# Optimization experiments

Measured on AMD Instinct MI355X. Metric: run time of the kernel, lower is better.

Reference implementation:

```python
import jax, jax.numpy as jnp
import numpy as np

EPS = 1e-08   # CanberraDistLayer eps (max(1e-8, 1e-8))
N_POW = 1.0   # similarity exponent
MAX_DIST = 1000000.0


def setup_inputs() -> dict:
    key = jax.random.key(0)
    k1, k2, k3, k4 = jax.random.split(key, 4)
    B, D_IN, H, OUT = 1024, 1024, 512, 512
    x = jax.random.normal(k1, (B, D_IN), dtype=jnp.float32)
    W1 = jax.random.normal(k2, (H, D_IN), dtype=jnp.float32) * 0.02  # MLP weight (torch Linear layout [out,in])
    b1 = jax.random.normal(k3, (H,), dtype=jnp.float32) * 0.02
    Wd = jax.random.normal(k4, (OUT, H), dtype=jnp.float32)          # dist-layer prototype rows
    return {"x": x, "W1": W1, "b1": b1, "Wd": Wd}


def reference(x, W1, b1, Wd):
    # MLP trunk: Linear + ReLU  -> hidden features h: [B, H]
    h = jax.nn.relu(jnp.einsum("bd,hd->bh", x, W1) + b1)
    # Canberra distance (variant='standard') of each hidden vector vs each weight row.
    # Broadcast to [B, OUT, H]; reduce over feature dim H.
    he = h[:, None, :]          # [B, 1, H]
    we = Wd[None, :, :]         # [1, OUT, H]
    numerator = jnp.abs(he - we)
    denominator = jnp.abs(he) + jnp.abs(we)
    denominator = jnp.where(denominator < EPS, EPS, denominator)
    canberra_dist = jnp.sum(numerator / denominator, axis=-1)  # [B, OUT]
    # scale=False path
    dist_clamped = jnp.clip(canberra_dist + EPS, EPS, MAX_DIST)
    similarity = dist_clamped ** (-N_POW)
    return similarity
```

## Files before the change

### kernel.cpp

```cpp
#include <hip/hip_runtime.h>
#include <hip/hip_fp16.h>

#define DIN 1024
#define H_SZ 512
#define OUT_SZ 512
#define EPSF 1e-8f

typedef __attribute__((ext_vector_type(8))) short short8v;
typedef __attribute__((ext_vector_type(4))) float f32x4;
typedef _Float16 half2v __attribute__((ext_vector_type(2)));

static __device__ inline void canb2f(unsigned hu, unsigned wu, unsigned& a) {
    unsigned mn, sm, y;
    asm("v_pk_min_f16 %0, %1, %2" : "=v"(mn) : "v"(hu), "v"(wu));
    asm("v_pk_add_f16 %0, %1, %2" : "=v"(sm) : "v"(hu), "v"(wu));
    y = 0x77997799u - sm;
    asm("v_pk_fma_f16 %0, %1, %2, %0" : "+v"(a) : "v"(mn), "v"(y));
}

static __device__ inline unsigned cvtpk(float lo, float hi) {
    unsigned u;
    asm("v_cvt_pk_bf16_f32 %0, %1, %2" : "=v"(u) : "v"(lo), "v"(hi));
    return u;
}

__global__ __launch_bounds__(512, 4) void gemm10(const float* __restrict__ x,
                                                 const float* __restrict__ W1,
                                                 const float* __restrict__ b1,
                                                 const float* __restrict__ Wd,
                                                 unsigned short* __restrict__ hh,
                                                 unsigned short* __restrict__ wh) {
    __shared__ unsigned short As[2][2][32][72];
    __shared__ unsigned short Bs[2][2][32][72];
    __shared__ float red[4][64][4];
    const int t  = threadIdx.x;

    const int flat = blockIdx.x + 32 * blockIdx.y;
    const int xcd  = flat & 7;
    const int idx  = flat >> 3;
    const int bt   = (xcd >> 1) * 8 + (idx & 7);
    const int ot   = (xcd & 1) * 8 + (idx >> 3);
    const int b0 = bt * 32;
    const int o0 = ot * 32;

    const int w  = t >> 6;
    const int l  = t & 63;
    const int q  = w & 3;
    const int kh = w >> 2;
    const int m0 = (q >> 1) * 16;
    const int n0 = (q & 1) * 16;
    const int lr = l & 15;
    const int lk = (l >> 4) * 8;
    const int th = t & 255;
    const int ar = th >> 3;
    const int ko = (th & 7) * 8;

    f32x4 acc = {0.f, 0.f, 0.f, 0.f};
    const float* arow = &x [(size_t)(b0 + ar) * DIN + kh * 512 + ko];
    const float* brow = &W1[(size_t)(o0 + ar) * DIN + kh * 512 + ko];

    float4 pa0[2], pa1[2], pb0[2], pb1[2];
    #pragma unroll
    for (int i = 0; i < 2; ++i) {
        pa0[i] = *reinterpret_cast<const float4*>(arow + i * 64);
        pa1[i] = *reinterpret_cast<const float4*>(arow + i * 64 + 4);
        pb0[i] = *reinterpret_cast<const float4*>(brow + i * 64);
        pb1[i] = *reinterpret_cast<const float4*>(brow + i * 64 + 4);
    }

    #pragma unroll
    for (int it = 0; it < 8; ++it) {
        const int sl  = it & 1;
        uint4 av, bv;
        av.x = cvtpk(pa0[sl].x, pa0[sl].y);
        av.y = cvtpk(pa0[sl].z, pa0[sl].w);
        av.z = cvtpk(pa1[sl].x, pa1[sl].y);
        av.w = cvtpk(pa1[sl].z, pa1[sl].w);
        bv.x = cvtpk(pb0[sl].x, pb0[sl].y);
        bv.y = cvtpk(pb0[sl].z, pb0[sl].w);
        bv.z = cvtpk(pb1[sl].x, pb1[sl].y);
        bv.w = cvtpk(pb1[sl].z, pb1[sl].w);
        *reinterpret_cast<uint4*>(&As[kh][sl][ar][ko]) = av;
        *reinterpret_cast<uint4*>(&Bs[kh][sl][ar][ko]) = bv;
        __syncthreads();
        if (it + 2 < 8) {
            pa0[sl] = *reinterpret_cast<const float4*>(arow + (it + 2) * 64);
            pa1[sl] = *reinterpret_cast<const float4*>(arow + (it + 2) * 64 + 4);
            pb0[sl] = *reinterpret_cast<const float4*>(brow + (it + 2) * 64);
            pb1[sl] = *reinterpret_cast<const float4*>(brow + (it + 2) * 64 + 4);
        }
        #pragma unroll
        for (int s = 0; s < 2; ++s) {
            const short8v af = *reinterpret_cast<const short8v*>(&As[kh][sl][m0 + lr][s * 32 + lk]);
            const short8v bf = *reinterpret_cast<const short8v*>(&Bs[kh][sl][n0 + lr][s * 32 + lk]);
            acc = __builtin_amdgcn_mfma_f32_16x16x32_bf16(af, bf, acc, 0, 0, 0);
        }
    }
    __syncthreads();
    if (kh == 1) {
        #pragma unroll
        for (int r = 0; r < 4; ++r) red[q][l][r] = acc[r];
    }
    __syncthreads();
    if (kh == 0) {
        const int col = o0 + n0 + lr;
        const float bias = b1[col];
        #pragma unroll
        for (int r = 0; r < 4; ++r) {
            const float v = acc[r] + red[q][l][r] + bias;
            const int m = b0 + m0 + (l >> 4) * 4 + r;
            hh[(size_t)m * H_SZ + col] = __half_as_ushort(__float2half(fmaxf(v, 0.0f)));
        }
    }
    const int gid = flat * 512 + t;
    const float wv0 = Wd[gid];
    wh[gid] = __half_as_ushort(__float2half(wv0 > 0.f ? wv0 : 0.f));
}

__global__ __launch_bounds__(512, 8) void canberra7(const unsigned short* __restrict__ hh,
                                                    const unsigned short* __restrict__ wh,
                                                    float* __restrict__ out) {
    __shared__ unsigned hs[32][132];
    __shared__ unsigned ws[16][132];
    const int t  = threadIdx.x;
    const int b0 = blockIdx.x * 32;
    const int o0 = blockIdx.y * 16;
    const unsigned* hu = reinterpret_cast<const unsigned*>(hh);
    const unsigned* wu = reinterpret_cast<const unsigned*>(wh);

    const int ks = t >> 6;
    const int l  = t & 63;
    const int bi = l >> 3;
    const int oj = l & 7;

    unsigned acc[4][2] = {};

    for (int ch = 0; ch < 2; ++ch) {
        if (ch) __syncthreads();
        #pragma unroll
        for (int r = 0; r < 2; ++r) {
            const int s = t + r * 512;
            const int row = s >> 5;
            const int c4  = s & 31;
            *reinterpret_cast<uint4*>(&hs[row][c4 * 4]) =
                *reinterpret_cast<const uint4*>(&hu[(size_t)(b0 + row) * 256 + ch * 128 + c4 * 4]);
        }
        {
            const int row = t >> 5;
            const int c4  = t & 31;
            *reinterpret_cast<uint4*>(&ws[row][c4 * 4]) =
                *reinterpret_cast<const uint4*>(&wu[(size_t)(o0 + row) * 256 + ch * 128 + c4 * 4]);
        }
        __syncthreads();

        #pragma unroll
        for (int g = 0; g < 4; ++g) {
            const int col = ks * 16 + g * 4;
            uint4 hv[4], wv[2];
            #pragma unroll
            for (int c = 0; c < 4; ++c)
                hv[c] = *reinterpret_cast<const uint4*>(&hs[bi + 8 * c][col]);
            #pragma unroll
            for (int d = 0; d < 2; ++d)
                wv[d] = *reinterpret_cast<const uint4*>(&ws[oj + 8 * d][col]);
            #pragma unroll
            for (int c = 0; c < 4; ++c) {
                #pragma unroll
                for (int d = 0; d < 2; ++d) {
                    canb2f(hv[c].x, wv[d].x, acc[c][d]);
                    canb2f(hv[c].y, wv[d].y, acc[c][d]);
                    canb2f(hv[c].z, wv[d].z, acc[c][d]);
                    canb2f(hv[c].w, wv[d].w, acc[c][d]);
                }
            }
        }
    }

    float p[8];
    #pragma unroll
    for (int c = 0; c < 4; ++c)
        #pragma unroll
        for (int d = 0; d < 2; ++d) {
            const half2v av = __builtin_bit_cast(half2v, acc[c][d]);
            p[c * 2 + d] = (float)av.x + (float)av.y;
        }

    __syncthreads();
    float* red = reinterpret_cast<float*>(&hs[0][0]);
    if (ks > 0) {
        const int slot = (ks - 1) * 64 + l;
        #pragma unroll
        for (int i = 0; i < 8; ++i) red[i * 448 + slot] = p[i];
    }
    __syncthreads();
    if (ks == 0) {
        #pragma unroll
        for (int q = 0; q < 7; ++q) {
            #pragma unroll
            for (int i = 0; i < 8; ++i) p[i] += red[i * 448 + q * 64 + l];
        }
        #pragma unroll
        for (int c = 0; c < 4; ++c) {
            #pragma unroll
            for (int d = 0; d < 2; ++d) {
                float dd = 512.0f - 2.0f * p[c * 2 + d] + EPSF;
                dd = fminf(fmaxf(dd, EPSF), 1000000.0f);
                out[(size_t)(b0 + bi + 8 * c) * OUT_SZ + o0 + oj + 8 * d] = 1.0f / dd;
            }
        }
    }
}

extern "C" void kernel_launch(void* const* d_in, const int* in_sizes, int n_in,
                              void* d_out, int out_size, void* d_ws, size_t ws_size,
                              hipStream_t stream) {
    const float* x  = (const float*)d_in[0];
    const float* W1 = (const float*)d_in[1];
    const float* b1 = (const float*)d_in[2];
    const float* Wd = (const float*)d_in[3];
    float* out = (float*)d_out;
    unsigned short* hh = (unsigned short*)d_ws;
    unsigned short* wh = (unsigned short*)((char*)d_ws + (1u << 20));

    gemm10<<<dim3(32, 16), 512, 0, stream>>>(x, W1, b1, Wd, hh, wh);
    canberra7<<<dim3(32, 32), 512, 0, stream>>>(hh, wh, out);
}
```

Baseline: 32.02 us.

## Load MFMA operands directly from global memory, dropping LDS staging and barriers

```diff
diff --git a/kernel.cpp b/kernel.cpp
--- a/kernel.cpp
+++ b/kernel.cpp
@@ -24,14 +24,12 @@
     return u;
 }
 
-__global__ __launch_bounds__(512, 4) void gemm10(const float* __restrict__ x,
+__global__ __launch_bounds__(512, 4) void gemm11(const float* __restrict__ x,
                                                  const float* __restrict__ W1,
                                                  const float* __restrict__ b1,
                                                  const float* __restrict__ Wd,
                                                  unsigned short* __restrict__ hh,
                                                  unsigned short* __restrict__ wh) {
-    __shared__ unsigned short As[2][2][32][72];
-    __shared__ unsigned short Bs[2][2][32][72];
     __shared__ float red[4][64][4];
     const int t  = threadIdx.x;
 
@@ -51,51 +49,28 @@
     const int n0 = (q & 1) * 16;
     const int lr = l & 15;
     const int lk = (l >> 4) * 8;
-    const int th = t & 255;
-    const int ar = th >> 3;
-    const int ko = (th & 7) * 8;
 
     f32x4 acc = {0.f, 0.f, 0.f, 0.f};
-    const float* arow = &x [(size_t)(b0 + ar) * DIN + kh * 512 + ko];
-    const float* brow = &W1[(size_t)(o0 + ar) * DIN + kh * 512 + ko];
-
-    float4 pa0[2], pa1[2], pb0[2], pb1[2];
+    const float4* pA = reinterpret_cast<const float4*>(
+        &x [(size_t)(b0 + m0 + lr) * DIN + kh * 512 + lk]);
+    const float4* pB = reinterpret_cast<const float4*>(
+        &W1[(size_t)(o0 + n0 + lr) * DIN + kh * 512 + lk]);
+
     #pragma unroll
-    for (int i = 0; i < 2; ++i) {
-        pa0[i] = *reinterpret_cast<const float4*>(arow + i * 64);
-        pa1[i] = *reinterpret_cast<const float4*>(arow + i * 64 + 4);
-        pb0[i] = *reinterpret_cast<const float4*>(brow + i * 64);
-        pb1[i] = *reinterpret_cast<const float4*>(brow + i * 64 + 4);
-    }
-
-    #pragma unroll
-    for (int it = 0; it < 8; ++it) {
-        const int sl  = it & 1;
+    for (int s = 0; s < 16; ++s) {
+        const float4 a0 = pA[s * 8];
+        const float4 a1 = pA[s * 8 + 1];
+        const float4 bq0 = pB[s * 8];
+        const float4 bq1 = pB[s * 8 + 1];
         uint4 av, bv;
-        av.x = cvtpk(pa0[sl].x, pa0[sl].y);
-        av.y = cvtpk(pa0[sl].z, pa0[sl].w);
-        av.z = cvtpk(pa1[sl].x, pa1[sl].y);
-        av.w = cvtpk(pa1[sl].z, pa1[sl].w);
-        bv.x = cvtpk(pb0[sl].x, pb0[sl].y);
-        bv.y = cvtpk(pb0[sl].z, pb0[sl].w);
-        bv.z = cvtpk(pb1[sl].x, pb1[sl].y);
-        bv.w = cvtpk(pb1[sl].z, pb1[sl].w);
-        *reinterpret_cast<uint4*>(&As[kh][sl][ar][ko]) = av;
-        *reinterpret_cast<uint4*>(&Bs[kh][sl][ar][ko]) = bv;
-        __syncthreads();
-        if (it + 2 < 8) {
-            pa0[sl] = *reinterpret_cast<const float4*>(arow + (it + 2) * 64);
-            pa1[sl] = *reinterpret_cast<const float4*>(arow + (it + 2) * 64 + 4);
-            pb0[sl] = *reinterpret_cast<const float4*>(brow + (it + 2) * 64);
-            pb1[sl] = *reinterpret_cast<const float4*>(brow + (it + 2) * 64 + 4);
-        }
-        #pragma unroll
-        for (int s = 0; s < 2; ++s) {
-            const short8v af = *reinterpret_cast<const short8v*>(&As[kh][sl][m0 + lr][s * 32 + lk]);
-            const short8v bf = *reinterpret_cast<const short8v*>(&Bs[kh][sl][n0 + lr][s * 32 + lk]);
-            acc = __builtin_amdgcn_mfma_f32_16x16x32_bf16(af, bf, acc, 0, 0, 0);
-        }
-    }
+        av.x = cvtpk(a0.x, a0.y);  av.y = cvtpk(a0.z, a0.w);
+        av.z = cvtpk(a1.x, a1.y);  av.w = cvtpk(a1.z, a1.w);
+        bv.x = cvtpk(bq0.x, bq0.y); bv.y = cvtpk(bq0.z, bq0.w);
+        bv.z = cvtpk(bq1.x, bq1.y); bv.w = cvtpk(bq1.z, bq1.w);
+        acc = __builtin_amdgcn_mfma_f32_16x16x32_bf16(
+            __builtin_bit_cast(short8v, av), __builtin_bit_cast(short8v, bv), acc, 0, 0, 0);
+    }
+
     __syncthreads();
     if (kh == 1) {
         #pragma unroll
@@ -222,6 +197,6 @@
     unsigned short* hh = (unsigned short*)d_ws;
     unsigned short* wh = (unsigned short*)((char*)d_ws + (1u << 20));
 
-    gemm10<<<dim3(32, 16), 512, 0, stream>>>(x, W1, b1, Wd, hh, wh);
+    gemm11<<<dim3(32, 16), 512, 0, stream>>>(x, W1, b1, Wd, hh, wh);
     canberra7<<<dim3(32, 32), 512, 0, stream>>>(hh, wh, out);
 }
```

New measurement: 54.52 us. 1.7x slower.
